# Performance work log

Hardware: AMD Instinct MI355X
Metric: run time of the kernel (lower is better)

## Reference

```python
import jax, jax.numpy as jnp
import numpy as np

B, C, H, W = 32, 384, 64, 64
M, R = 64, 16  # token_count, factor_r


def setup_inputs() -> dict:
    key = jax.random.key(0)
    k1, k2, k3, k4 = jax.random.split(key, 4)
    x = jax.random.normal(k1, (B, C, H, W), dtype=jnp.float32)
    # 1x1 conv == per-pixel linear map C -> R
    Vw = jax.random.normal(k2, (R, C), dtype=jnp.float32) * (1.0 / np.sqrt(C))
    Vb = jax.random.normal(k3, (R,), dtype=jnp.float32) * 0.01
    U = jax.random.normal(k4, (M, R), dtype=jnp.float32) * 0.02
    return {"x": x, "Vw": Vw, "Vb": Vb, "U": U}


def reference(x, Vw, Vb, U):
    b, c, h, w = x.shape
    n = h * w
    x_flat = x.reshape(b, c, n)                       # [B,C,N]
    # 1x1 conv projection: [B,R,N]
    V = jnp.einsum('rc,bcn->brn', Vw, x_flat) + Vb[None, :, None]
    # low-rank bilinear logits: [B,M,N]
    L = jnp.einsum('mr,brn->bmn', U, V)
    # softmax over token dim (axis=1), matching F.softmax(L, dim=1)
    S = jax.nn.softmax(L, axis=1)
    # pooled tokens: [B,C,M]
    T = jnp.einsum('bcn,bmn->bcm', x_flat, S)
    return (T, S)
```

## Files before the change

kernel.cpp:

```cpp
#include <hip/hip_runtime.h>
#include <hip/hip_bf16.h>

#define B_ 32
#define C_ 384
#define N_ 4096
#define M_ 64
#define R_ 16

typedef __attribute__((ext_vector_type(8))) short short8;
typedef __attribute__((ext_vector_type(4))) float f32x4;
typedef __attribute__((ext_vector_type(4))) int i32x4;

static __device__ __forceinline__ unsigned short f2bf(float f) {
    union { float f; unsigned u; } v; v.f = f;
    unsigned r = v.u + 0x7fffu + ((v.u >> 16) & 1u);
    return (unsigned short)(r >> 16);
}

__global__ __launch_bounds__(256) void k_w2(
    const float* __restrict__ Vw, const float* __restrict__ Vb,
    const float* __restrict__ U, unsigned short* __restrict__ W2,
    float* __restrict__ b2)
{
    __shared__ float vws[16 * 384];
    __shared__ float vbs[16];
    const int t = threadIdx.x;

    #pragma unroll
    for (int j = 0; j < 6; ++j)
        ((float4*)vws)[t + j * 256] = ((const float4*)Vw)[t + j * 256];
    if (t < 16) vbs[t] = Vb[t];
    __syncthreads();

    const int m  = blockIdx.x * 8 + (t >> 5);
    const int cg = t & 31;
    float u[R_];
    #pragma unroll
    for (int r = 0; r < R_; ++r) u[r] = U[m * R_ + r];
    if (cg == 0) {
        float a = 0.f;
        #pragma unroll
        for (int r = 0; r < R_; ++r) a = fmaf(u[r], vbs[r], a);
        b2[m] = a;
    }
    #pragma unroll
    for (int j = 0; j < 6; ++j) {
        const int c = cg * 2 + j * 64;
        float a0 = 0.f, a1 = 0.f;
        #pragma unroll
        for (int r = 0; r < R_; ++r) {
            float2 vv = *(const float2*)(vws + r * C_ + c);
            a0 = fmaf(u[r], vv.x, a0);
            a1 = fmaf(u[r], vv.y, a1);
        }
        unsigned pk = (unsigned)f2bf(a0) | ((unsigned)f2bf(a1) << 16);
        *(unsigned*)&W2[m * C_ + c] = pk;
    }
}

__global__ __launch_bounds__(512, 2) void k_fused(
    const float* __restrict__ x, const unsigned short* __restrict__ W2,
    const float* __restrict__ b2g, float* __restrict__ S, float* __restrict__ T)
{
    __shared__ unsigned short xcn[C_ * 128];
    __shared__ union {
        unsigned short xts[128][68];
        unsigned short slds[M_ * 128];
    } uu;
    __shared__ float wred[2][4][128];

    const int t    = threadIdx.x;
    const int lane = t & 63;
    const int col  = lane & 15;
    const int q    = lane >> 4;
    const int w    = t >> 6;
    const int g    = w >> 1;
    const int h    = w & 1;

    const int b  = blockIdx.x >> 3;
    const int nq = blockIdx.x & 7;

    short8 af1[12];
    #pragma unroll
    for (int kk = 0; kk < 12; ++kk)
        af1[kk] = *(const short8*)(W2 + (g * 16 + col) * C_ + kk * 32 + q * 8);

    float bias[4];
    #pragma unroll
    for (int r = 0; r < 4; ++r) bias[r] = b2g[g * 16 + q * 4 + r];

    f32x4 acc2[3][4];
    #pragma unroll
    for (int ci = 0; ci < 3; ++ci)
        #pragma unroll
        for (int mt = 0; mt < 4; ++mt) acc2[ci][mt] = (f32x4){0.f, 0.f, 0.f, 0.f};

    const float* xb = x + (size_t)b * C_ * N_ + nq * 512 + 2 * lane;

    float2 xv[2][8];
    auto issue = [&](float2 (&dst)[8], int sub_, int kc_) {
        const float* xp = xb + (size_t)(kc_ * 64 + w * 8) * N_ + sub_ * 128;
        #pragma unroll
        for (int i = 0; i < 8; ++i)
            dst[i] = *(const float2*)(xp + (size_t)i * N_);
    };

    issue(xv[0], 0, 0);

    for (int sub = 0; sub < 4; ++sub) {
        f32x4 acc1[4];
        #pragma unroll
        for (int nt = 0; nt < 4; ++nt) acc1[nt] = (f32x4){0.f, 0.f, 0.f, 0.f};

        #pragma unroll
        for (int kc = 0; kc < 6; ++kc) {
            if (kc < 5) issue(xv[(kc + 1) & 1], sub, kc + 1);
            {
                float2 (&v)[8] = xv[kc & 1];
                unsigned short bx[8], by[8];
                #pragma unroll
                for (int i = 0; i < 8; ++i) { bx[i] = f2bf(v[i].x); by[i] = f2bf(v[i].y); }
                #pragma unroll
                for (int i = 0; i < 8; ++i) {
                    int c = kc * 64 + w * 8 + i;
                    unsigned pk = (unsigned)bx[i] | ((unsigned)by[i] << 16);
                    *(unsigned*)((char*)xcn + c * 256 + ((lane * 4) ^ ((c & 7) << 4))) = pk;
                }
                i32x4 pa, pb;
                #pragma unroll
                for (int j = 0; j < 4; ++j) {
                    pa[j] = (int)((unsigned)bx[2 * j] | ((unsigned)bx[2 * j + 1] << 16));
                    pb[j] = (int)((unsigned)by[2 * j] | ((unsigned)by[2 * j + 1] << 16));
                }
                *(i32x4*)&uu.xts[2 * lane][w * 8]     = pa;
                *(i32x4*)&uu.xts[2 * lane + 1][w * 8] = pb;
            }
            __syncthreads();
            #pragma unroll
            for (int ks = 0; ks < 2; ++ks) {
                short8 bfr[4];
                #pragma unroll
                for (int nt = 0; nt < 4; ++nt)
                    bfr[nt] = *(const short8*)&uu.xts[h * 64 + nt * 16 + col][ks * 32 + q * 8];
                #pragma unroll
                for (int nt = 0; nt < 4; ++nt)
                    acc1[nt] = __builtin_amdgcn_mfma_f32_16x16x32_bf16(
                        af1[kc * 2 + ks], bfr[nt], acc1[nt], 0, 0, 0);
            }
            __syncthreads();
        }

        #pragma unroll
        for (int nt = 0; nt < 4; ++nt) {
            float mx = -3.4e38f;
            #pragma unroll
            for (int r = 0; r < 4; ++r) {
                float vv = acc1[nt][r] + bias[r];
                acc1[nt][r] = vv;
                mx = fmaxf(mx, vv);
            }
            mx = fmaxf(mx, __shfl_xor(mx, 16, 64));
            mx = fmaxf(mx, __shfl_xor(mx, 32, 64));
            if (q == 0) wred[0][g][h * 64 + nt * 16 + col] = mx;
        }
        __syncthreads();
        #pragma unroll
        for (int nt = 0; nt < 4; ++nt) {
            int n = h * 64 + nt * 16 + col;
            float gm = fmaxf(fmaxf(wred[0][0][n], wred[0][1][n]),
                             fmaxf(wred[0][2][n], wred[0][3][n]));
            float s = 0.f;
            #pragma unroll
            for (int r = 0; r < 4; ++r) {
                float e = __expf(acc1[nt][r] - gm);
                acc1[nt][r] = e;
                s += e;
            }
            s += __shfl_xor(s, 16, 64);
            s += __shfl_xor(s, 32, 64);
            if (q == 0) wred[1][g][n] = s;
        }
        __syncthreads();
        float inv_[4];
        #pragma unroll
        for (int nt = 0; nt < 4; ++nt) {
            int n = h * 64 + nt * 16 + col;
            float ts = (wred[1][0][n] + wred[1][1][n]) + (wred[1][2][n] + wred[1][3][n]);
            inv_[nt] = 1.0f / ts;
        }

        if (sub < 3) issue(xv[0], sub + 1, 0);

        float* Sp = S + (size_t)(b * M_ + g * 16 + q * 4) * N_ + nq * 512 + sub * 128;
        #pragma unroll
        for (int nt = 0; nt < 4; ++nt) {
            int n = h * 64 + nt * 16 + col;
            #pragma unroll
            for (int r = 0; r < 4; ++r) {
                float p = acc1[nt][r] * inv_[nt];
                Sp[(size_t)r * N_ + n] = p;
                int m = g * 16 + q * 4 + r;
                *(unsigned short*)((char*)uu.slds + m * 256 + ((2 * n) ^ ((m & 7) << 4))) = f2bf(p);
            }
        }
        __syncthreads();

        #pragma unroll
        for (int ks = 0; ks < 4; ++ks) {
            short8 a2[3], bsf[4];
            #pragma unroll
            for (int ci = 0; ci < 3; ++ci) {
                int c = w * 48 + ci * 16 + col;
                a2[ci] = *(const short8*)((char*)xcn + c * 256 +
                                          ((ks * 64 + q * 16) ^ ((c & 7) << 4)));
            }
            #pragma unroll
            for (int mt = 0; mt < 4; ++mt) {
                int m = mt * 16 + col;
                bsf[mt] = *(const short8*)((char*)uu.slds + m * 256 +
                                           ((ks * 64 + q * 16) ^ ((m & 7) << 4)));
            }
            #pragma unroll
            for (int ci = 0; ci < 3; ++ci)
                #pragma unroll
                for (int mt = 0; mt < 4; ++mt)
                    acc2[ci][mt] = __builtin_amdgcn_mfma_f32_16x16x32_bf16(
                        a2[ci], bsf[mt], acc2[ci][mt], 0, 0, 0);
        }
        __syncthreads();
    }

    float* Tb = T + (size_t)b * C_ * M_;
    #pragma unroll
    for (int ci = 0; ci < 3; ++ci) {
        int c = w * 48 + ci * 16 + q * 4;
        #pragma unroll
        for (int mt = 0; mt < 4; ++mt)
            #pragma unroll
            for (int r = 0; r < 4; ++r)
                atomicAdd(&Tb[(size_t)(c + r) * M_ + mt * 16 + col], acc2[ci][mt][r]);
    }
}

extern "C" void kernel_launch(void* const* d_in, const int* in_sizes, int n_in,
                              void* d_out, int out_size, void* d_ws, size_t ws_size,
                              hipStream_t stream) {
    const float* x  = (const float*)d_in[0];
    const float* Vw = (const float*)d_in[1];
    const float* Vb = (const float*)d_in[2];
    const float* U  = (const float*)d_in[3];
    float* T = (float*)d_out;
    float* S = (float*)d_out + (size_t)B_ * C_ * M_;

    unsigned short* W2 = (unsigned short*)d_ws;
    float* b2 = (float*)((char*)d_ws + 64 * 384 * 2);

    hipMemsetAsync(T, 0, (size_t)B_ * C_ * M_ * sizeof(float), stream);
    k_w2<<<dim3(8), dim3(256), 0, stream>>>(Vw, Vb, U, W2, b2);
    k_fused<<<dim3(256), dim3(512), 0, stream>>>(x, W2, b2, S, T);
}
```

Measured before the change: 318.5 us.

## Deepen x prefetch, double-buffer xts, and merge softmax reduction passes

The global load prefetch of x grows from two register buffers to three, so loads run further ahead, and the loads for the next sub-tile are issued during the last kc iterations. The transposed LDS tile is double-buffered and no longer shares storage with slds, which removes one barrier per kc step. The softmax now computes each group's local max and sum in one pass and rescales them with exp corrections, dropping one block barrier. In exchange, register pressure and LDS use both rise, which could reduce occupancy below the two blocks per CU the launch bounds request.

```diff
diff --git a/kernel.cpp b/kernel.cpp
--- a/kernel.cpp
+++ b/kernel.cpp
@@ -63,10 +63,8 @@
     const float* __restrict__ b2g, float* __restrict__ S, float* __restrict__ T)
 {
     __shared__ unsigned short xcn[C_ * 128];
-    __shared__ union {
-        unsigned short xts[128][68];
-        unsigned short slds[M_ * 128];
-    } uu;
+    __shared__ unsigned short xts[2][128][68];
+    __shared__ unsigned short slds[M_ * 128];
     __shared__ float wred[2][4][128];
 
     const int t    = threadIdx.x;
@@ -97,51 +95,59 @@
 
     const float* xb = x + (size_t)b * C_ * N_ + nq * 512 + 2 * lane;
 
-    float2 xv[2][8];
-    auto issue = [&](float2 (&dst)[8], int sub_, int kc_) {
-        const float* xp = xb + (size_t)(kc_ * 64 + w * 8) * N_ + sub_ * 128;
+    float2 xv[3][8];
+
+    auto ISSUE = [&](float2 (&dst)[8], int subp, int kcp) {
+        const float* xp = xb + (size_t)(kcp * 64 + w * 8) * N_ + subp * 128;
         #pragma unroll
         for (int i = 0; i < 8; ++i)
             dst[i] = *(const float2*)(xp + (size_t)i * N_);
     };
 
-    issue(xv[0], 0, 0);
+    auto CONVERT = [&](float2 (&v)[8], int kcp, int buf) {
+        unsigned short bx[8], by[8];
+        #pragma unroll
+        for (int i = 0; i < 8; ++i) { bx[i] = f2bf(v[i].x); by[i] = f2bf(v[i].y); }
+        #pragma unroll
+        for (int i = 0; i < 8; ++i) {
+            int c = kcp * 64 + w * 8 + i;
+            unsigned pk = (unsigned)bx[i] | ((unsigned)by[i] << 16);
+            *(unsigned*)((char*)xcn + c * 256 + ((lane * 4) ^ ((c & 7) << 4))) = pk;
+        }
+        i32x4 pa, pb;
+        #pragma unroll
+        for (int j = 0; j < 4; ++j) {
+            pa[j] = (int)((unsigned)bx[2 * j] | ((unsigned)bx[2 * j + 1] << 16));
+            pb[j] = (int)((unsigned)by[2 * j] | ((unsigned)by[2 * j + 1] << 16));
+        }
+        *(i32x4*)&xts[buf][2 * lane][w * 8]     = pa;
+        *(i32x4*)&xts[buf][2 * lane + 1][w * 8] = pb;
+    };
+
+    ISSUE(xv[0], 0, 0);
+    ISSUE(xv[1], 0, 1);
+    ISSUE(xv[2], 0, 2);
 
     for (int sub = 0; sub < 4; ++sub) {
         f32x4 acc1[4];
         #pragma unroll
         for (int nt = 0; nt < 4; ++nt) acc1[nt] = (f32x4){0.f, 0.f, 0.f, 0.f};
 
+        CONVERT(xv[0], 0, 0);
+        __syncthreads();
+
         #pragma unroll
         for (int kc = 0; kc < 6; ++kc) {
-            if (kc < 5) issue(xv[(kc + 1) & 1], sub, kc + 1);
-            {
-                float2 (&v)[8] = xv[kc & 1];
-                unsigned short bx[8], by[8];
-                #pragma unroll
-                for (int i = 0; i < 8; ++i) { bx[i] = f2bf(v[i].x); by[i] = f2bf(v[i].y); }
-                #pragma unroll
-                for (int i = 0; i < 8; ++i) {
-                    int c = kc * 64 + w * 8 + i;
-                    unsigned pk = (unsigned)bx[i] | ((unsigned)by[i] << 16);
-                    *(unsigned*)((char*)xcn + c * 256 + ((lane * 4) ^ ((c & 7) << 4))) = pk;
-                }
-                i32x4 pa, pb;
-                #pragma unroll
-                for (int j = 0; j < 4; ++j) {
-                    pa[j] = (int)((unsigned)bx[2 * j] | ((unsigned)bx[2 * j + 1] << 16));
-                    pb[j] = (int)((unsigned)by[2 * j] | ((unsigned)by[2 * j + 1] << 16));
-                }
-                *(i32x4*)&uu.xts[2 * lane][w * 8]     = pa;
-                *(i32x4*)&uu.xts[2 * lane + 1][w * 8] = pb;
-            }
-            __syncthreads();
+            if (kc < 5) CONVERT(xv[(kc + 1) % 3], kc + 1, (kc + 1) & 1);
+            if (kc < 3)          ISSUE(xv[kc % 3], sub, kc + 3);
+            else if (sub < 3)    ISSUE(xv[kc % 3], sub + 1, kc - 3);
+
             #pragma unroll
             for (int ks = 0; ks < 2; ++ks) {
                 short8 bfr[4];
                 #pragma unroll
                 for (int nt = 0; nt < 4; ++nt)
-                    bfr[nt] = *(const short8*)&uu.xts[h * 64 + nt * 16 + col][ks * 32 + q * 8];
+                    bfr[nt] = *(const short8*)&xts[kc & 1][h * 64 + nt * 16 + col][ks * 32 + q * 8];
                 #pragma unroll
                 for (int nt = 0; nt < 4; ++nt)
                     acc1[nt] = __builtin_amdgcn_mfma_f32_16x16x32_bf16(
@@ -150,6 +156,7 @@
             __syncthreads();
         }
 
+        float mxl[4];
         #pragma unroll
         for (int nt = 0; nt < 4; ++nt) {
             float mx = -3.4e38f;
@@ -161,46 +168,46 @@
             }
             mx = fmaxf(mx, __shfl_xor(mx, 16, 64));
             mx = fmaxf(mx, __shfl_xor(mx, 32, 64));
-            if (q == 0) wred[0][g][h * 64 + nt * 16 + col] = mx;
-        }
-        __syncthreads();
+            float s = 0.f;
+            #pragma unroll
+            for (int r = 0; r < 4; ++r) {
+                float e = __expf(acc1[nt][r] - mx);
+                acc1[nt][r] = e;
+                s += e;
+            }
+            s += __shfl_xor(s, 16, 64);
+            s += __shfl_xor(s, 32, 64);
+            mxl[nt] = mx;
+            if (q == 0) {
+                int n = h * 64 + nt * 16 + col;
+                wred[0][g][n] = mx;
+                wred[1][g][n] = s;
+            }
+        }
+        __syncthreads();
+
+        float scl[4];
         #pragma unroll
         for (int nt = 0; nt < 4; ++nt) {
             int n = h * 64 + nt * 16 + col;
-            float gm = fmaxf(fmaxf(wred[0][0][n], wred[0][1][n]),
-                             fmaxf(wred[0][2][n], wred[0][3][n]));
-            float s = 0.f;
-            #pragma unroll
-            for (int r = 0; r < 4; ++r) {
-                float e = __expf(acc1[nt][r] - gm);
-                acc1[nt][r] = e;
-                s += e;
-            }
-            s += __shfl_xor(s, 16, 64);
-            s += __shfl_xor(s, 32, 64);
-            if (q == 0) wred[1][g][n] = s;
-        }
-        __syncthreads();
-        float inv_[4];
+            float m0 = wred[0][0][n], m1 = wred[0][1][n];
+            float m2 = wred[0][2][n], m3 = wred[0][3][n];
+            float M  = fmaxf(fmaxf(m0, m1), fmaxf(m2, m3));
+            float tot = wred[1][0][n] * __expf(m0 - M) + wred[1][1][n] * __expf(m1 - M)
+                      + wred[1][2][n] * __expf(m2 - M) + wred[1][3][n] * __expf(m3 - M);
+            scl[nt] = __expf(mxl[nt] - M) / tot;
+        }
+
+        float* Sp = S + (size_t)(b * M_ + g * 16 + q * 4) * N_ + nq * 512 + sub * 128;
         #pragma unroll
         for (int nt = 0; nt < 4; ++nt) {
             int n = h * 64 + nt * 16 + col;
-            float ts = (wred[1][0][n] + wred[1][1][n]) + (wred[1][2][n] + wred[1][3][n]);
-            inv_[nt] = 1.0f / ts;
-        }
-
-        if (sub < 3) issue(xv[0], sub + 1, 0);
-
-        float* Sp = S + (size_t)(b * M_ + g * 16 + q * 4) * N_ + nq * 512 + sub * 128;
-        #pragma unroll
-        for (int nt = 0; nt < 4; ++nt) {
-            int n = h * 64 + nt * 16 + col;
             #pragma unroll
             for (int r = 0; r < 4; ++r) {
-                float p = acc1[nt][r] * inv_[nt];
+                float p = acc1[nt][r] * scl[nt];
                 Sp[(size_t)r * N_ + n] = p;
                 int m = g * 16 + q * 4 + r;
-                *(unsigned short*)((char*)uu.slds + m * 256 + ((2 * n) ^ ((m & 7) << 4))) = f2bf(p);
+                *(unsigned short*)((char*)slds + m * 256 + ((2 * n) ^ ((m & 7) << 4))) = f2bf(p);
             }
         }
         __syncthreads();
@@ -217,7 +224,7 @@
             #pragma unroll
             for (int mt = 0; mt < 4; ++mt) {
                 int m = mt * 16 + col;
-                bsf[mt] = *(const short8*)((char*)uu.slds + m * 256 +
+                bsf[mt] = *(const short8*)((char*)slds + m * 256 +
                                            ((ks * 64 + q * 16) ^ ((m & 7) << 4)));
             }
             #pragma unroll
```

Result: faster. 310.5 us (-2.5%).
